# Optimization experiments

Measured on AMD Instinct MI355X. Metric: run time of the kernel, lower is better.

The kernel has to match this reference:

```python
import jax, jax.numpy as jnp
import numpy as np

IN_DIM = 128
OUT_DIM = 128
ATTN_DIM = 64
N_REL = 200
N_NODE = 50000
N_EDGE = 500000
N_QUERY = 64
COE_TIMEDIFF = 0.2  # computed in torch code but unused downstream


def setup_inputs() -> dict:
    key = jax.random.key(0)
    ks = jax.random.split(key, 24)
    # edges: [E,7] with columns (r_idx, _, rel, _, tau, sub, obj)
    r_idx = jax.random.randint(ks[0], (N_EDGE,), 0, N_QUERY)
    rel = jax.random.randint(ks[1], (N_EDGE,), 0, 2 * N_REL + 1)
    tau = jax.random.randint(ks[2], (N_EDGE,), -1, 366)  # -1 triggers the where() fallback
    sub = jax.random.randint(ks[3], (N_EDGE,), 0, N_NODE)
    obj = jax.random.randint(ks[4], (N_EDGE,), 0, N_NODE)
    fill = jnp.zeros((N_EDGE,), jnp.int64 if jax.config.jax_enable_x64 else jnp.int32)
    edges = jnp.stack([r_idx, fill, rel, fill, tau, sub, obj], axis=1)
    s = 1.0 / np.sqrt(IN_DIM)
    sa = 1.0 / np.sqrt(ATTN_DIM)
    return {
        "q_sub": jax.random.randint(ks[5], (N_QUERY,), 0, N_NODE),
        "q_rel": jax.random.randint(ks[6], (N_QUERY,), 0, 2 * N_REL + 1),
        "q_tau": jax.random.randint(ks[7], (N_QUERY,), 0, 366),
        "hidden": jax.random.normal(ks[8], (N_NODE, IN_DIM), jnp.float32),
        "edges": edges,
        "n_node": N_NODE,
        "old_nodes_new_idx": jax.random.randint(ks[9], (10000,), 0, N_NODE),
        "rela_embed": jax.random.normal(ks[10], (2 * N_REL + 1, IN_DIM), jnp.float32),
        "Ws": jax.random.normal(ks[11], (IN_DIM, ATTN_DIM), jnp.float32) * s,
        "Wr": jax.random.normal(ks[12], (IN_DIM, ATTN_DIM), jnp.float32) * s,
        "Wqr_W": jax.random.normal(ks[13], (IN_DIM, ATTN_DIM), jnp.float32) * s,
        "Wqr_b": jax.random.normal(ks[14], (ATTN_DIM,), jnp.float32) * s,
        "Wtau": jax.random.normal(ks[15], (IN_DIM, ATTN_DIM), jnp.float32) * s,
        "w_alpha_W": jax.random.normal(ks[16], (ATTN_DIM, 1), jnp.float32) * sa,
        "w_alpha_b": jax.random.normal(ks[17], (1,), jnp.float32) * sa,
        "Wh": jax.random.normal(ks[18], (IN_DIM, OUT_DIM), jnp.float32) * s,
        "wt1": jax.random.normal(ks[19], (1, IN_DIM), jnp.float32),
        "bt1": jax.random.normal(ks[20], (1, IN_DIM), jnp.float32),
        "wt2": jax.random.normal(ks[21], (1, IN_DIM), jnp.float32),
        "bt2": jax.random.normal(ks[22], (1, IN_DIM), jnp.float32),
    }


def reference(q_sub, q_rel, q_tau, hidden, edges, n_node, old_nodes_new_idx,
              rela_embed, Ws, Wr, Wqr_W, Wqr_b, Wtau, w_alpha_W, w_alpha_b,
              Wh, wt1, bt1, wt2, bt2):
    r_idx = edges[:, 0]
    rel = edges[:, 2]
    tau = edges[:, 4]
    sub = edges[:, 5]
    obj = edges[:, 6]
    hs = hidden[sub]                      # [E, in_dim] gather
    hr = rela_embed[rel]                  # [E, in_dim]
    h_qr = rela_embed[q_rel][r_idx]       # [E, in_dim]
    taus_q = q_tau[r_idx]
    tau = jnp.where(tau >= 0, tau, taus_q)
    delta_tau = (tau - taus_q).astype(hidden.dtype)[:, None]  # [E,1]
    h_tau = wt1 * delta_tau + bt1 + jnp.sin(wt2 * delta_tau + bt2)  # [E, in_dim]
    message = hs + hr + h_tau
    pre = jax.nn.relu(hs @ Ws + hr @ Wr + (h_qr @ Wqr_W + Wqr_b) + h_tau @ Wtau)
    alpha = jax.nn.sigmoid(pre @ w_alpha_W + w_alpha_b)  # [E,1]
    msg_agg = jax.ops.segment_sum(alpha * message, obj, num_segments=n_node)
    return msg_agg @ Wh  # act is identity by default
```

## Files before the change

kernel.cpp:

```cpp
#include <hip/hip_runtime.h>
#include <hip/hip_fp16.h>

#define IN_DIM   128
#define OUT_DIM  128
#define ATTN_DIM 64
#define N_RELV   401
#define N_NODE   50000
#define N_EDGE   500000
#define N_QUERY  64
#define N_DT     731
#define CAP      40

#define NBW_NODE 782
#define NBW_REL  7
#define NBW_DT   12
#define NBW_QR   1
#define NBW_ZERO 13
#define RB0      NBW_NODE
#define DB0      (NBW_NODE + NBW_REL)
#define QB0      (DB0 + NBW_DT)
#define ZB0      (QB0 + NBW_QR)
#define FB0      (ZB0 + NBW_ZERO)
#define NB_TOT   (FB0 + 1)

typedef unsigned short ushort_t;
typedef unsigned int   uint_t;
typedef __attribute__((ext_vector_type(8))) short v8s;
typedef __attribute__((ext_vector_type(4))) float v4f;

__device__ __forceinline__ int clampi(int v, int lo, int hi) {
    return v < lo ? lo : (v > hi ? hi : v);
}
__device__ __forceinline__ float bu2f(ushort_t u) {
    union { uint_t i; float f; } v; v.i = ((uint_t)u) << 16; return v.f;
}
__device__ __forceinline__ float blo(uint_t u) { return bu2f((ushort_t)(u & 0xffff)); }
__device__ __forceinline__ float bhi(uint_t u) { return bu2f((ushort_t)(u >> 16)); }
__device__ __forceinline__ uint_t cvtpk(float a, float b) {
    uint_t r;
    asm("v_cvt_pk_bf16_f32 %0, %1, %2" : "=v"(r) : "v"(a), "v"(b));
    return r;
}

__device__ __forceinline__ int swz_byte(int row, int byte_in_row) {
    return (row * 256 + byte_in_row) ^ ((row & 7) << 4);
}

__device__ __forceinline__ void stage_w64(ushort_t* shw, const float* __restrict__ W,
                                          int tid) {
    #pragma unroll
    for (int i = 0; i < 4; ++i) {
        const int pi = tid + 256 * i;
        const int kp = pi >> 4;
        const int n4 = (pi & 15) * 4;
        const float4 A = *(const float4*)(W + (size_t)(2 * kp) * 64 + n4);
        const float4 B = *(const float4*)(W + (size_t)(2 * kp + 1) * 64 + n4);
        const float Aa[4] = {A.x, A.y, A.z, A.w};
        const float Ba[4] = {B.x, B.y, B.z, B.w};
        #pragma unroll
        for (int j = 0; j < 4; ++j)
            *(uint_t*)((char*)shw + swz_byte(n4 + j, kp * 4)) = cvtpk(Aa[j], Ba[j]);
    }
}
__device__ __forceinline__ void stage_w128(ushort_t* shw, const float* __restrict__ W,
                                           int tid) {
    #pragma unroll
    for (int i = 0; i < 8; ++i) {
        const int pi = tid + 256 * i;
        const int kp = pi >> 5;
        const int n4 = (pi & 31) * 4;
        const float4 A = *(const float4*)(W + (size_t)(2 * kp) * 128 + n4);
        const float4 B = *(const float4*)(W + (size_t)(2 * kp + 1) * 128 + n4);
        const float Aa[4] = {A.x, A.y, A.z, A.w};
        const float Ba[4] = {B.x, B.y, B.z, B.w};
        #pragma unroll
        for (int j = 0; j < 4; ++j)
            *(uint_t*)((char*)shw + swz_byte(64 + n4 + j, kp * 4)) = cvtpk(Aa[j], Ba[j]);
    }
}
__device__ __forceinline__ void load_x_rows(const float* __restrict__ X, int rowc,
                                            int q, v8s hfr[4]) {
    #pragma unroll
    for (int c = 0; c < 4; ++c) {
        const float4 f0 = *(const float4*)(X + (size_t)rowc * 128 + 32 * c + 8 * q);
        const float4 f1 = *(const float4*)(X + (size_t)rowc * 128 + 32 * c + 8 * q + 4);
        union { v8s s; uint4 u; } uu;
        uu.u = make_uint4(cvtpk(f0.x, f0.y), cvtpk(f0.z, f0.w),
                          cvtpk(f1.x, f1.y), cvtpk(f1.z, f1.w));
        hfr[c] = uu.s;
    }
}
__device__ __forceinline__ void mfma_store(const ushort_t* shw, const v8s hfr[4],
                                           int row, int Nlim,
                                           ushort_t* __restrict__ attn_out,
                                           ushort_t* __restrict__ msg_out,
                                           int m16, int q) {
    #pragma unroll
    for (int t = 0; t < 12; ++t) {
        v4f acc = {0.f, 0.f, 0.f, 0.f};
        #pragma unroll
        for (int c = 0; c < 4; ++c) {
            const v8s wfr = *(const v8s*)((const char*)shw +
                              swz_byte(16 * t + m16, (32 * c + 8 * q) * 2));
            acc = __builtin_amdgcn_mfma_f32_16x16x32_bf16(wfr, hfr[c], acc, 0, 0, 0);
        }
        if (row < Nlim) {
            const uint_t u0 = cvtpk(acc[0], acc[1]);
            const uint_t u1 = cvtpk(acc[2], acc[3]);
            const int dim = 16 * t + 4 * q;
            if (dim < 64)
                *(uint2*)(attn_out + (size_t)row * 64 + dim) = make_uint2(u0, u1);
            else
                *(uint2*)(msg_out + (size_t)row * 128 + (dim - 64)) = make_uint2(u0, u1);
        }
    }
}

__global__ __launch_bounds__(256) void fused_pre(
    const float* __restrict__ hidden, const float* __restrict__ Ws,
    const float* __restrict__ Wh,   const float* __restrict__ rela,
    const float* __restrict__ Wr,   const float* __restrict__ Wtau,
    const float* __restrict__ wt1,  const float* __restrict__ bt1,
    const float* __restrict__ wt2,  const float* __restrict__ bt2,
    const int* __restrict__ q_rel,  const float* __restrict__ WqrW,
    const float* __restrict__ Wqrb, const int* __restrict__ edges,
    ushort_t* __restrict__ node_attn, ushort_t* __restrict__ node_msg,
    ushort_t* __restrict__ rel_attn,  ushort_t* __restrict__ rel_msg,
    ushort_t* __restrict__ dt_attn,   ushort_t* __restrict__ dt_msg,
    ushort_t* __restrict__ Xqr,
    int* __restrict__ flag, int* __restrict__ cnt, int* __restrict__ ovfn)
{
    __shared__ ushort_t shw[192 * 128];
    const int bid = blockIdx.x, tid = threadIdx.x;
    const int wid = tid >> 6, lane = tid & 63;
    const int m16 = lane & 15, q = lane >> 4;

    if (bid < NBW_NODE) {
        stage_w64 (shw, Ws, tid);
        stage_w128(shw, Wh, tid);
        __syncthreads();
        const int row  = bid * 64 + wid * 16 + m16;
        const int rowc = row < N_NODE ? row : N_NODE - 1;
        v8s hfr[4];
        load_x_rows(hidden, rowc, q, hfr);
        mfma_store(shw, hfr, row, N_NODE, node_attn, node_msg, m16, q);
    } else if (bid < DB0) {
        stage_w64 (shw, Wr, tid);
        stage_w128(shw, Wh, tid);
        __syncthreads();
        const int row  = (bid - RB0) * 64 + wid * 16 + m16;
        const int rowc = row < N_RELV ? row : N_RELV - 1;
        v8s hfr[4];
        load_x_rows(rela, rowc, q, hfr);
        mfma_store(shw, hfr, row, N_RELV, rel_attn, rel_msg, m16, q);
    } else if (bid < QB0) {
        stage_w64 (shw, Wtau, tid);
        stage_w128(shw, Wh, tid);
        __syncthreads();
        const int row  = (bid - DB0) * 64 + wid * 16 + m16;
        const int rowc = row < N_DT ? row : N_DT - 1;
        const float dtv = (float)(rowc - 365);
        v8s hfr[4];
        #pragma unroll
        for (int c = 0; c < 4; ++c) {
            const int o = 32 * c + 8 * q;
            const float4 w1a = *(const float4*)(wt1 + o), w1b = *(const float4*)(wt1 + o + 4);
            const float4 b1a = *(const float4*)(bt1 + o), b1b = *(const float4*)(bt1 + o + 4);
            const float4 w2a = *(const float4*)(wt2 + o), w2b = *(const float4*)(wt2 + o + 4);
            const float4 b2a = *(const float4*)(bt2 + o), b2b = *(const float4*)(bt2 + o + 4);
            const float h0 = w1a.x * dtv + b1a.x + sinf(w2a.x * dtv + b2a.x);
            const float h1 = w1a.y * dtv + b1a.y + sinf(w2a.y * dtv + b2a.y);
            const float h2 = w1a.z * dtv + b1a.z + sinf(w2a.z * dtv + b2a.z);
            const float h3 = w1a.w * dtv + b1a.w + sinf(w2a.w * dtv + b2a.w);
            const float h4 = w1b.x * dtv + b1b.x + sinf(w2b.x * dtv + b2b.x);
            const float h5 = w1b.y * dtv + b1b.y + sinf(w2b.y * dtv + b2b.y);
            const float h6 = w1b.z * dtv + b1b.z + sinf(w2b.z * dtv + b2b.z);
            const float h7 = w1b.w * dtv + b1b.w + sinf(w2b.w * dtv + b2b.w);
            union { v8s s; uint4 u; } uu;
            uu.u = make_uint4(cvtpk(h0, h1), cvtpk(h2, h3), cvtpk(h4, h5), cvtpk(h6, h7));
            hfr[c] = uu.s;
        }
        mfma_store(shw, hfr, row, N_DT, dt_attn, dt_msg, m16, q);
    } else if (bid < ZB0) {
        int* ok = (int*)shw;
        if (tid == 0) *ok = 1;
        __syncthreads();
        int badv = 0;
        for (int t = tid; t < 1000; t += 256) {
            const int w = edges[2 * t + 1];
            if (w != 0 && w != -1) badv = 1;
        }
        if (badv) *ok = 0;
        __syncthreads();
        const int i64 = *ok;
        __syncthreads();

        stage_w64(shw, WqrW, tid);
        __syncthreads();
        const int qrow = wid * 16 + m16;
        const int relq = clampi(q_rel[i64 ? 2 * qrow : qrow], 0, N_RELV - 1);
        v8s hfr[4];
        load_x_rows(rela, relq, q, hfr);
        #pragma unroll
        for (int t = 0; t < 4; ++t) {
            v4f acc = {0.f, 0.f, 0.f, 0.f};
            #pragma unroll
            for (int c = 0; c < 4; ++c) {
                const v8s wfr = *(const v8s*)((const char*)shw +
                                  swz_byte(16 * t + m16, (32 * c + 8 * q) * 2));
                acc = __builtin_amdgcn_mfma_f32_16x16x32_bf16(wfr, hfr[c], acc, 0, 0, 0);
            }
            const int dim = 16 * t + 4 * q;
            const float4 bi = *(const float4*)(Wqrb + dim);
            const uint_t u0 = cvtpk(acc[0] + bi.x, acc[1] + bi.y);
            const uint_t u1 = cvtpk(acc[2] + bi.z, acc[3] + bi.w);
            *(uint2*)(Xqr + (size_t)qrow * 64 + dim) = make_uint2(u0, u1);
        }
    } else if (bid < FB0) {
        int4* c4 = (int4*)cnt;
        const int b = (bid - ZB0) * 256 + tid;
        #pragma unroll
        for (int k = 0; k < 4; ++k) {
            const int i4 = b * 4 + k;
            if (i4 < N_NODE / 4) c4[i4] = make_int4(0, 0, 0, 0);
        }
    } else {
        int* ok = (int*)shw;
        if (tid == 0) *ok = 0;
        __syncthreads();
        int badv = 0;
        for (int t = tid; t < 1000; t += 256) {
            const int w = edges[2 * t + 1];
            if (w != 0 && w != -1) badv = 1;
        }
        if (badv) *ok = 1;
        __syncthreads();
        if (tid == 0) { flag[0] = (*ok == 0) ? 1 : 0; ovfn[0] = 0; }
    }
}

__device__ __forceinline__ float dot8(uint4 xs, uint4 xr, uint4 xt, uint4 xq,
                                      float4 wA, float4 wB)
{
    float s0, s1, v;
    s0 = blo(xs.x) + blo(xr.x) + blo(xt.x) + blo(xq.x);
    s1 = bhi(xs.x) + bhi(xr.x) + bhi(xt.x) + bhi(xq.x);
    v  = fmaxf(s0, 0.f) * wA.x + fmaxf(s1, 0.f) * wA.y;
    s0 = blo(xs.y) + blo(xr.y) + blo(xt.y) + blo(xq.y);
    s1 = bhi(xs.y) + bhi(xr.y) + bhi(xt.y) + bhi(xq.y);
    v += fmaxf(s0, 0.f) * wA.z + fmaxf(s1, 0.f) * wA.w;
    s0 = blo(xs.z) + blo(xr.z) + blo(xt.z) + blo(xq.z);
    s1 = bhi(xs.z) + bhi(xr.z) + bhi(xt.z) + bhi(xq.z);
    v += fmaxf(s0, 0.f) * wB.x + fmaxf(s1, 0.f) * wB.y;
    s0 = blo(xs.w) + blo(xr.w) + blo(xt.w) + blo(xq.w);
    s1 = bhi(xs.w) + bhi(xr.w) + bhi(xt.w) + bhi(xq.w);
    v += fmaxf(s0, 0.f) * wB.z + fmaxf(s1, 0.f) * wB.w;
    return v;
}

__global__ __launch_bounds__(256) void alpha_scatter(
    const int* __restrict__ edges, const int* __restrict__ q_tau,
    const ushort_t* __restrict__ node_attn, const ushort_t* __restrict__ rel_attn,
    const ushort_t* __restrict__ dt_attn,  const ushort_t* __restrict__ Xqr,
    const float* __restrict__ w_alpha_W, const float* __restrict__ w_alpha_b,
    const int* __restrict__ flag, int* __restrict__ cnt,
    int2* __restrict__ meta, int* __restrict__ ovfn, int4* __restrict__ ovfl)
{
    const int g   = threadIdx.x & 7;
    const int grp = threadIdx.x >> 3;
    const int e0r = blockIdx.x * 128 + grp * 4;
    const int e0  = e0r <= N_EDGE - 4 ? e0r : N_EDGE - 4;
    const int i64 = flag[0];

    const float4 wA = *(const float4*)(w_alpha_W + 8 * g);
    const float4 wB = *(const float4*)(w_alpha_W + 8 * g + 4);

    int r0, rel0, tau0, sub0, obj0, r1, rel1, tau1, sub1, obj1;
    int r2, rel2, tau2, sub2, obj2, r3, rel3, tau3, sub3, obj3;
    if (!i64) {
        const int4 ev = *(const int4*)(edges + (size_t)e0 * 7 + 4 * (g < 6 ? g : 6));
        #define GETF(j) __shfl(((j) & 3) == 0 ? ev.x : ((j) & 3) == 1 ? ev.y : \
                               ((j) & 3) == 2 ? ev.z : ev.w, (j) >> 2, 8)
        r0 = GETF(0);  rel0 = GETF(2);  tau0 = GETF(4);  sub0 = GETF(5);  obj0 = GETF(6);
        r1 = GETF(7);  rel1 = GETF(9);  tau1 = GETF(11); sub1 = GETF(12); obj1 = GETF(13);
        r2 = GETF(14); rel2 = GETF(16); tau2 = GETF(18); sub2 = GETF(19); obj2 = GETF(20);
        r3 = GETF(21); rel3 = GETF(23); tau3 = GETF(25); sub3 = GETF(26); obj3 = GETF(27);
        #undef GETF
    } else {
        const int* E0 = edges + (size_t)(e0    ) * 14;
        const int* E1 = edges + (size_t)(e0 + 1) * 14;
        const int* E2 = edges + (size_t)(e0 + 2) * 14;
        const int* E3 = edges + (size_t)(e0 + 3) * 14;
        r0 = E0[0]; rel0 = E0[4]; tau0 = E0[8]; sub0 = E0[10]; obj0 = E0[12];
        r1 = E1[0]; rel1 = E1[4]; tau1 = E1[8]; sub1 = E1[10]; obj1 = E1[12];
        r2 = E2[0]; rel2 = E2[4]; tau2 = E2[8]; sub2 = E2[10]; obj2 = E2[12];
        r3 = E3[0]; rel3 = E3[4]; tau3 = E3[8]; sub3 = E3[10]; obj3 = E3[12];
    }
    r0 = clampi(r0, 0, N_QUERY - 1); rel0 = clampi(rel0, 0, N_RELV - 1);
    sub0 = clampi(sub0, 0, N_NODE - 1); obj0 = clampi(obj0, 0, N_NODE - 1);
    r1 = clampi(r1, 0, N_QUERY - 1); rel1 = clampi(rel1, 0, N_RELV - 1);
    sub1 = clampi(sub1, 0, N_NODE - 1); obj1 = clampi(obj1, 0, N_NODE - 1);
    r2 = clampi(r2, 0, N_QUERY - 1); rel2 = clampi(rel2, 0, N_RELV - 1);
    sub2 = clampi(sub2, 0, N_NODE - 1); obj2 = clampi(obj2, 0, N_NODE - 1);
    r3 = clampi(r3, 0, N_QUERY - 1); rel3 = clampi(rel3, 0, N_RELV - 1);
    sub3 = clampi(sub3, 0, N_NODE - 1); obj3 = clampi(obj3, 0, N_NODE - 1);

    const int tq0 = q_tau[i64 ? 2 * r0 : r0];
    const int tq1 = q_tau[i64 ? 2 * r1 : r1];
    const int tq2 = q_tau[i64 ? 2 * r2 : r2];
    const int tq3 = q_tau[i64 ? 2 * r3 : r3];
    if (tau0 < 0) tau0 = tq0;
    if (tau1 < 0) tau1 = tq1;
    if (tau2 < 0) tau2 = tq2;
    if (tau3 < 0) tau3 = tq3;
    const int di0 = clampi(tau0 - tq0 + 365, 0, N_DT - 1);
    const int di1 = clampi(tau1 - tq1 + 365, 0, N_DT - 1);
    const int di2 = clampi(tau2 - tq2 + 365, 0, N_DT - 1);
    const int di3 = clampi(tau3 - tq3 + 365, 0, N_DT - 1);

    const uint4 xs0 = *(const uint4*)(node_attn + (size_t)sub0 * ATTN_DIM + 8 * g);
    const uint4 xr0 = *(const uint4*)(rel_attn + (size_t)rel0 * ATTN_DIM + 8 * g);
    const uint4 xt0 = *(const uint4*)(dt_attn  + (size_t)di0  * ATTN_DIM + 8 * g);
    const uint4 xq0 = *(const uint4*)(Xqr      + (size_t)r0   * ATTN_DIM + 8 * g);
    const uint4 xs1 = *(const uint4*)(node_attn + (size_t)sub1 * ATTN_DIM + 8 * g);
    const uint4 xr1 = *(const uint4*)(rel_attn + (size_t)rel1 * ATTN_DIM + 8 * g);
    const uint4 xt1 = *(const uint4*)(dt_attn  + (size_t)di1  * ATTN_DIM + 8 * g);
    const uint4 xq1 = *(const uint4*)(Xqr      + (size_t)r1   * ATTN_DIM + 8 * g);
    const uint4 xs2 = *(const uint4*)(node_attn + (size_t)sub2 * ATTN_DIM + 8 * g);
    const uint4 xr2 = *(const uint4*)(rel_attn + (size_t)rel2 * ATTN_DIM + 8 * g);
    const uint4 xt2 = *(const uint4*)(dt_attn  + (size_t)di2  * ATTN_DIM + 8 * g);
    const uint4 xq2 = *(const uint4*)(Xqr      + (size_t)r2   * ATTN_DIM + 8 * g);
    const uint4 xs3 = *(const uint4*)(node_attn + (size_t)sub3 * ATTN_DIM + 8 * g);
    const uint4 xr3 = *(const uint4*)(rel_attn + (size_t)rel3 * ATTN_DIM + 8 * g);
    const uint4 xt3 = *(const uint4*)(dt_attn  + (size_t)di3  * ATTN_DIM + 8 * g);
    const uint4 xq3 = *(const uint4*)(Xqr      + (size_t)r3   * ATTN_DIM + 8 * g);

    float v0 = dot8(xs0, xr0, xt0, xq0, wA, wB);
    float v1 = dot8(xs1, xr1, xt1, xq1, wA, wB);
    float v2 = dot8(xs2, xr2, xt2, xq2, wA, wB);
    float v3 = dot8(xs3, xr3, xt3, xq3, wA, wB);

    #pragma unroll
    for (int off = 4; off > 0; off >>= 1) {
        v0 += __shfl_xor(v0, off, 8);
        v1 += __shfl_xor(v1, off, 8);
        v2 += __shfl_xor(v2, off, 8);
        v3 += __shfl_xor(v3, off, 8);
    }

    if (g < 4 && e0r + g < N_EDGE) {
        const float vg  = g == 0 ? v0 : (g == 1 ? v1 : (g == 2 ? v2 : v3));
        const int objg  = g == 0 ? obj0 : (g == 1 ? obj1 : (g == 2 ? obj2 : obj3));
        const int subg  = g == 0 ? sub0 : (g == 1 ? sub1 : (g == 2 ? sub2 : sub3));
        const int dig   = g == 0 ? di0  : (g == 1 ? di1  : (g == 2 ? di2  : di3));
        const int relg  = g == 0 ? rel0 : (g == 1 ? rel1 : (g == 2 ? rel2 : rel3));
        const float alpha = 1.f / (1.f + __expf(-(vg + w_alpha_b[0])));
        const int pos = atomicAdd(&cnt[objg], 1);
        if (pos < CAP) {
            const uint_t px = (uint_t)subg | ((uint_t)dig << 17) | ((uint_t)(relg & 31) << 27);
            const uint_t py = (uint_t)(relg >> 5) |
                              ((uint_t)__half_as_ushort(__float2half_rn(alpha)) << 16);
            meta[(size_t)pos * N_NODE + objg] = make_int2((int)px, (int)py);
        } else {
            const int ov = atomicAdd(ovfn, 1);
            if (ov < N_EDGE)
                ovfl[ov] = make_int4(subg | (dig << 17), relg | (objg << 9),
                                     __float_as_int(alpha), 0);
        }
    }
}

__device__ __forceinline__ void gather3(
    int2 m, int l16,
    const ushort_t* __restrict__ node_msg, const ushort_t* __restrict__ rel_msg,
    const ushort_t* __restrict__ dt_msg,
    uint4& A, uint4& B, uint4& T, float& al)
{
    const int sub = m.x & 0x1FFFF;
    const int di  = ((uint_t)m.x >> 17) & 0x3FF;
    const int rel = (((uint_t)m.x >> 27) & 31) | (((uint_t)m.y & 0xF) << 5);
    al = __half2float(__ushort_as_half((ushort_t)((uint_t)m.y >> 16)));
    A = *(const uint4*)(node_msg + (size_t)sub * 128 + 8 * l16);
    B = *(const uint4*)(rel_msg  + (size_t)rel * 128 + 8 * l16);
    T = *(const uint4*)(dt_msg   + (size_t)di  * 128 + 8 * l16);
}
__device__ __forceinline__ void accum8(
    uint4 A, uint4 B, uint4 T, float al,
    float& a0, float& a1, float& a2, float& a3,
    float& a4, float& a5, float& a6, float& a7)
{
    a0 += al * (blo(A.x) + blo(B.x) + blo(T.x));
    a1 += al * (bhi(A.x) + bhi(B.x) + bhi(T.x));
    a2 += al * (blo(A.y) + blo(B.y) + blo(T.y));
    a3 += al * (bhi(A.y) + bhi(B.y) + bhi(T.y));
    a4 += al * (blo(A.z) + blo(B.z) + blo(T.z));
    a5 += al * (bhi(A.z) + bhi(B.z) + bhi(T.z));
    a6 += al * (blo(A.w) + blo(B.w) + blo(T.w));
    a7 += al * (bhi(A.w) + bhi(B.w) + bhi(T.w));
}

__global__ __launch_bounds__(256) void agg_kernel(
    const int* __restrict__ cnt, const int2* __restrict__ meta,
    const int* __restrict__ ovfn, const int4* __restrict__ ovfl,
    const ushort_t* __restrict__ node_msg, const ushort_t* __restrict__ rel_msg,
    const ushort_t* __restrict__ dt_msg, float* __restrict__ out)
{
    const int lane = threadIdx.x & 63;
    const int sg   = lane >> 4;
    const int l16  = lane & 15;
    const int n    = blockIdx.x * 4 + (threadIdx.x >> 6);

    int m = cnt[n]; if (m > CAP) m = CAP;
    float a0 = 0.f, a1 = 0.f, a2 = 0.f, a3 = 0.f;
    float a4 = 0.f, a5 = 0.f, a6 = 0.f, a7 = 0.f;

    int j = 0;
    for (; j + 7 < m; j += 8) {
        const int2 ma = meta[(size_t)(j     + sg) * N_NODE + n];
        const int2 mb = meta[(size_t)(j + 4 + sg) * N_NODE + n];
        uint4 Aa, Ba, Ta; float wa; gather3(ma, l16, node_msg, rel_msg, dt_msg, Aa, Ba, Ta, wa);
        uint4 Ab, Bb, Tb; float wb; gather3(mb, l16, node_msg, rel_msg, dt_msg, Ab, Bb, Tb, wb);
        accum8(Aa, Ba, Ta, wa, a0, a1, a2, a3, a4, a5, a6, a7);
        accum8(Ab, Bb, Tb, wb, a0, a1, a2, a3, a4, a5, a6, a7);
    }
    for (; j < m; j += 4) {
        if (j + sg < m) {
            const int2 ma = meta[(size_t)(j + sg) * N_NODE + n];
            uint4 Aa, Ba, Ta; float wa; gather3(ma, l16, node_msg, rel_msg, dt_msg, Aa, Ba, Ta, wa);
            accum8(Aa, Ba, Ta, wa, a0, a1, a2, a3, a4, a5, a6, a7);
        }
    }

    int nov = ovfn[0]; if (nov > N_EDGE) nov = N_EDGE;
    for (int i = 0; i < nov; ++i) {
        const int4 mo = ovfl[i];
        const int objo = (int)((uint_t)mo.y >> 9);
        if (objo != n || sg != 0) continue;
        const int subo = mo.x & 0x1FFFF;
        const int dio  = (int)((uint_t)mo.x >> 17);
        const int relo = mo.y & 0x1FF;
        const float alo = __int_as_float(mo.z);
        const uint4 A = *(const uint4*)(node_msg + (size_t)subo * 128 + 8 * l16);
        const uint4 B = *(const uint4*)(rel_msg  + (size_t)relo * 128 + 8 * l16);
        const uint4 T = *(const uint4*)(dt_msg   + (size_t)dio  * 128 + 8 * l16);
        accum8(A, B, T, alo, a0, a1, a2, a3, a4, a5, a6, a7);
    }

    a0 += __shfl_xor(a0, 16, 64); a0 += __shfl_xor(a0, 32, 64);
    a1 += __shfl_xor(a1, 16, 64); a1 += __shfl_xor(a1, 32, 64);
    a2 += __shfl_xor(a2, 16, 64); a2 += __shfl_xor(a2, 32, 64);
    a3 += __shfl_xor(a3, 16, 64); a3 += __shfl_xor(a3, 32, 64);
    a4 += __shfl_xor(a4, 16, 64); a4 += __shfl_xor(a4, 32, 64);
    a5 += __shfl_xor(a5, 16, 64); a5 += __shfl_xor(a5, 32, 64);
    a6 += __shfl_xor(a6, 16, 64); a6 += __shfl_xor(a6, 32, 64);
    a7 += __shfl_xor(a7, 16, 64); a7 += __shfl_xor(a7, 32, 64);

    if (sg == 0) {
        float4 o0; o0.x = a0; o0.y = a1; o0.z = a2; o0.w = a3;
        float4 o1; o1.x = a4; o1.y = a5; o1.z = a6; o1.w = a7;
        *(float4*)(out + (size_t)n * OUT_DIM + 8 * l16)     = o0;
        *(float4*)(out + (size_t)n * OUT_DIM + 8 * l16 + 4) = o1;
    }
}

__device__ __forceinline__ void parse_edge(const int* __restrict__ edges, int e,
                                           int i64, int& r, int& rel, int& tau,
                                           int& sub, int& obj) {
    if (i64) {
        const int* E = edges + (size_t)e * 14;
        r = E[0]; rel = E[4]; tau = E[8]; sub = E[10]; obj = E[12];
    } else {
        const int* E = edges + (size_t)e * 7;
        r = E[0]; rel = E[2]; tau = E[4]; sub = E[5]; obj = E[6];
    }
    r   = clampi(r,   0, N_QUERY - 1);
    rel = clampi(rel, 0, N_RELV - 1);
    sub = clampi(sub, 0, N_NODE - 1);
    obj = clampi(obj, 0, N_NODE - 1);
}

__global__ __launch_bounds__(256) void edge_atomic_kernel(
    const int* __restrict__ edges, const int* __restrict__ q_tau,
    const ushort_t* __restrict__ node_attn, const ushort_t* __restrict__ node_msg,
    const ushort_t* __restrict__ rel_attn,  const ushort_t* __restrict__ rel_msg,
    const ushort_t* __restrict__ dt_attn,   const ushort_t* __restrict__ dt_msg,
    const ushort_t* __restrict__ Xqr,
    const float* __restrict__ w_alpha_W, const float* __restrict__ w_alpha_b,
    const int* __restrict__ flag, float* __restrict__ out)
{
    const int lane = threadIdx.x & 63;
    const int e    = blockIdx.x * 4 + (threadIdx.x >> 6);
    const int i64  = flag[0];

    int r, rel, tau, sub, obj;
    parse_edge(edges, e, i64, r, rel, tau, sub, obj);
    const int tq = q_tau[i64 ? 2 * r : r];
    if (tau < 0) tau = tq;
    const int di = clampi(tau - tq + 365, 0, N_DT - 1);

    const float xs = bu2f(node_attn[(size_t)sub * ATTN_DIM + lane]);
    const float xr = bu2f(rel_attn[(size_t)rel * ATTN_DIM + lane]);
    const float xt = bu2f(dt_attn[(size_t)di  * ATTN_DIM + lane]);
    const float xq = bu2f(Xqr[(size_t)r * ATTN_DIM + lane]);

    float v = fmaxf(xs + xr + xq + xt, 0.f) * w_alpha_W[lane];
    #pragma unroll
    for (int off = 32; off > 0; off >>= 1)
        v += __shfl_down(v, off, 64);
    v = __shfl(v, 0, 64);
    const float alpha = 1.f / (1.f + __expf(-(v + w_alpha_b[0])));

    const uint_t am = *(const uint_t*)(node_msg + (size_t)sub * 128 + 2 * lane);
    const uint_t bm = *(const uint_t*)(rel_msg  + (size_t)rel * 128 + 2 * lane);
    const uint_t tm = *(const uint_t*)(dt_msg   + (size_t)di  * 128 + 2 * lane);
    const float mx = blo(am) + blo(bm) + blo(tm);
    const float my = bhi(am) + bhi(bm) + bhi(tm);

    float* dst = out + (size_t)obj * OUT_DIM;
    atomicAdd(dst + 2 * lane,     alpha * mx);
    atomicAdd(dst + 2 * lane + 1, alpha * my);
}

extern "C" void kernel_launch(void* const* d_in, const int* in_sizes, int n_in,
                              void* d_out, int out_size, void* d_ws, size_t ws_size,
                              hipStream_t stream)
{
    const int*   q_rel  = (const int*)d_in[1];
    const int*   q_tau  = (const int*)d_in[2];
    const float* hidden = (const float*)d_in[3];
    const int*   edges  = (const int*)d_in[4];
    const float* rela   = (const float*)d_in[7];
    const float* Ws     = (const float*)d_in[8];
    const float* Wr     = (const float*)d_in[9];
    const float* WqrW   = (const float*)d_in[10];
    const float* Wqrb   = (const float*)d_in[11];
    const float* Wtau   = (const float*)d_in[12];
    const float* waW    = (const float*)d_in[13];
    const float* wab    = (const float*)d_in[14];
    const float* Wh     = (const float*)d_in[15];
    const float* wt1    = (const float*)d_in[16];
    const float* bt1    = (const float*)d_in[17];
    const float* wt2    = (const float*)d_in[18];
    const float* bt2    = (const float*)d_in[19];
    float* out = (float*)d_out;

    char* p = (char*)d_ws;
    size_t off = 0;
    auto carve = [&](size_t bytes) {
        char* q = p + off;
        off = (off + bytes + 255) & ~(size_t)255;
        return q;
    };
    int*      flag      = (int*)     carve(64);
    int*      cnt       = (int*)     carve((size_t)N_NODE * 4);
    int*      ovfn      = (int*)     carve(64);
    ushort_t* XqrB      = (ushort_t*)carve((size_t)N_QUERY * ATTN_DIM * 2);
    ushort_t* rel_attn  = (ushort_t*)carve((size_t)N_RELV * ATTN_DIM * 2);
    ushort_t* rel_msg   = (ushort_t*)carve((size_t)N_RELV * OUT_DIM * 2);
    ushort_t* dt_attn   = (ushort_t*)carve((size_t)N_DT * ATTN_DIM * 2);
    ushort_t* dt_msg    = (ushort_t*)carve((size_t)N_DT * OUT_DIM * 2);
    ushort_t* node_attn = (ushort_t*)carve((size_t)N_NODE * ATTN_DIM * 2);
    ushort_t* node_msg  = (ushort_t*)carve((size_t)N_NODE * OUT_DIM * 2);
    int2*     meta      = (int2*)    carve((size_t)N_NODE * CAP * 8);
    int4*     ovfl      = (int4*)    carve((size_t)N_EDGE * 16);
    const size_t need_full = off;

    fused_pre<<<NB_TOT, 256, 0, stream>>>(
        hidden, Ws, Wh, rela, Wr, Wtau, wt1, bt1, wt2, bt2,
        q_rel, WqrW, Wqrb, edges,
        node_attn, node_msg, rel_attn, rel_msg, dt_attn, dt_msg, XqrB,
        flag, cnt, ovfn);

    if (ws_size >= need_full) {
        alpha_scatter<<<(N_EDGE + 127) / 128, 256, 0, stream>>>(
            edges, q_tau, node_attn, rel_attn, dt_attn, XqrB,
            waW, wab, flag, cnt, meta, ovfn, ovfl);
        agg_kernel<<<N_NODE / 4, 256, 0, stream>>>(cnt, meta, ovfn, ovfl,
                                                   node_msg, rel_msg, dt_msg, out);
    } else {
        (void)hipMemsetAsync(out, 0, (size_t)out_size * sizeof(float), stream);
        edge_atomic_kernel<<<N_EDGE / 4, 256, 0, stream>>>(edges, q_tau,
                                                           node_attn, node_msg,
                                                           rel_attn, rel_msg,
                                                           dt_attn, dt_msg, XqrB,
                                                           waW, wab, flag, out);
    }
}
```

Baseline: 193.5 us.

## Stage query tables in LDS and swizzle agg block order across XCDs

Measured after the change: 193.1 us. About the same (-0.2%).

```diff
diff --git a/kernel.cpp b/kernel.cpp
--- a/kernel.cpp
+++ b/kernel.cpp
@@ -266,14 +266,30 @@
     const int* __restrict__ flag, int* __restrict__ cnt,
     int2* __restrict__ meta, int* __restrict__ ovfn, int4* __restrict__ ovfl)
 {
-    const int g   = threadIdx.x & 7;
-    const int grp = threadIdx.x >> 3;
+    __shared__ uint_t lXqr[N_QUERY * 32];
+    __shared__ int    lTq[N_QUERY];
+
+    const int tid = threadIdx.x;
+    const int i64 = flag[0];
+
+    {
+        const int r = tid >> 2, p = tid & 3;
+        const uint4 a = *(const uint4*)(Xqr + (size_t)r * ATTN_DIM + p * 16);
+        const uint4 b = *(const uint4*)(Xqr + (size_t)r * ATTN_DIM + p * 16 + 8);
+        *(uint4*)(lXqr + r * 32 + p * 8)     = a;
+        *(uint4*)(lXqr + r * 32 + p * 8 + 4) = b;
+    }
+    if (tid < N_QUERY) lTq[tid] = q_tau[i64 ? 2 * tid : tid];
+    __syncthreads();
+
+    const int g   = tid & 7;
+    const int grp = tid >> 3;
     const int e0r = blockIdx.x * 128 + grp * 4;
     const int e0  = e0r <= N_EDGE - 4 ? e0r : N_EDGE - 4;
-    const int i64 = flag[0];
 
     const float4 wA = *(const float4*)(w_alpha_W + 8 * g);
     const float4 wB = *(const float4*)(w_alpha_W + 8 * g + 4);
+    const float  wb = w_alpha_b[0];
 
     int r0, rel0, tau0, sub0, obj0, r1, rel1, tau1, sub1, obj1;
     int r2, rel2, tau2, sub2, obj2, r3, rel3, tau3, sub3, obj3;
@@ -305,10 +321,10 @@
     r3 = clampi(r3, 0, N_QUERY - 1); rel3 = clampi(rel3, 0, N_RELV - 1);
     sub3 = clampi(sub3, 0, N_NODE - 1); obj3 = clampi(obj3, 0, N_NODE - 1);
 
-    const int tq0 = q_tau[i64 ? 2 * r0 : r0];
-    const int tq1 = q_tau[i64 ? 2 * r1 : r1];
-    const int tq2 = q_tau[i64 ? 2 * r2 : r2];
-    const int tq3 = q_tau[i64 ? 2 * r3 : r3];
+    const int tq0 = lTq[r0];
+    const int tq1 = lTq[r1];
+    const int tq2 = lTq[r2];
+    const int tq3 = lTq[r3];
     if (tau0 < 0) tau0 = tq0;
     if (tau1 < 0) tau1 = tq1;
     if (tau2 < 0) tau2 = tq2;
@@ -321,19 +337,21 @@
     const uint4 xs0 = *(const uint4*)(node_attn + (size_t)sub0 * ATTN_DIM + 8 * g);
     const uint4 xr0 = *(const uint4*)(rel_attn + (size_t)rel0 * ATTN_DIM + 8 * g);
     const uint4 xt0 = *(const uint4*)(dt_attn  + (size_t)di0  * ATTN_DIM + 8 * g);
-    const uint4 xq0 = *(const uint4*)(Xqr      + (size_t)r0   * ATTN_DIM + 8 * g);
     const uint4 xs1 = *(const uint4*)(node_attn + (size_t)sub1 * ATTN_DIM + 8 * g);
     const uint4 xr1 = *(const uint4*)(rel_attn + (size_t)rel1 * ATTN_DIM + 8 * g);
     const uint4 xt1 = *(const uint4*)(dt_attn  + (size_t)di1  * ATTN_DIM + 8 * g);
-    const uint4 xq1 = *(const uint4*)(Xqr      + (size_t)r1   * ATTN_DIM + 8 * g);
     const uint4 xs2 = *(const uint4*)(node_attn + (size_t)sub2 * ATTN_DIM + 8 * g);
     const uint4 xr2 = *(const uint4*)(rel_attn + (size_t)rel2 * ATTN_DIM + 8 * g);
     const uint4 xt2 = *(const uint4*)(dt_attn  + (size_t)di2  * ATTN_DIM + 8 * g);
-    const uint4 xq2 = *(const uint4*)(Xqr      + (size_t)r2   * ATTN_DIM + 8 * g);
     const uint4 xs3 = *(const uint4*)(node_attn + (size_t)sub3 * ATTN_DIM + 8 * g);
     const uint4 xr3 = *(const uint4*)(rel_attn + (size_t)rel3 * ATTN_DIM + 8 * g);
     const uint4 xt3 = *(const uint4*)(dt_attn  + (size_t)di3  * ATTN_DIM + 8 * g);
-    const uint4 xq3 = *(const uint4*)(Xqr      + (size_t)r3   * ATTN_DIM + 8 * g);
+    const uint4 xq0 = *(const uint4*)(lXqr + r0 * 32 + 4 * g);
+    const uint4 xq1 = *(const uint4*)(lXqr + r1 * 32 + 4 * g);
+    const uint4 xq2 = *(const uint4*)(lXqr + r2 * 32 + 4 * g);
+    const uint4 xq3 = *(const uint4*)(lXqr + r3 * 32 + 4 * g);
+
+    __builtin_amdgcn_sched_barrier(0);
 
     float v0 = dot8(xs0, xr0, xt0, xq0, wA, wB);
     float v1 = dot8(xs1, xr1, xt1, xq1, wA, wB);
@@ -354,7 +372,7 @@
         const int subg  = g == 0 ? sub0 : (g == 1 ? sub1 : (g == 2 ? sub2 : sub3));
         const int dig   = g == 0 ? di0  : (g == 1 ? di1  : (g == 2 ? di2  : di3));
         const int relg  = g == 0 ? rel0 : (g == 1 ? rel1 : (g == 2 ? rel2 : rel3));
-        const float alpha = 1.f / (1.f + __expf(-(vg + w_alpha_b[0])));
+        const float alpha = 1.f / (1.f + __expf(-(vg + wb)));
         const int pos = atomicAdd(&cnt[objg], 1);
         if (pos < CAP) {
             const uint_t px = (uint_t)subg | ((uint_t)dig << 17) | ((uint_t)(relg & 31) << 27);
@@ -405,10 +423,16 @@
     const ushort_t* __restrict__ node_msg, const ushort_t* __restrict__ rel_msg,
     const ushort_t* __restrict__ dt_msg, float* __restrict__ out)
 {
+    const int nblk = gridDim.x;
+    const int bq = nblk >> 3, br = nblk & 7;
+    const int xcd = blockIdx.x & 7, idx = blockIdx.x >> 3;
+    const int bswz = (xcd < br ? xcd * (bq + 1)
+                               : br * (bq + 1) + (xcd - br) * bq) + idx;
+
     const int lane = threadIdx.x & 63;
     const int sg   = lane >> 4;
     const int l16  = lane & 15;
-    const int n    = blockIdx.x * 4 + (threadIdx.x >> 6);
+    const int n    = bswz * 4 + (threadIdx.x >> 6);
 
     int m = cnt[n]; if (m > CAP) m = CAP;
     float a0 = 0.f, a1 = 0.f, a2 = 0.f, a3 = 0.f;
```
